# Optimization experiments

Measured on AMD Instinct MI355X. Metric: run time of the kernel, lower is better.

Reference implementation:

```python
import jax, jax.numpy as jnp
import numpy as np

B, P, K = 32, 2048, 20   # events, points per event, kNN neighbors
EPS = 1e-5               # BatchNorm eps (eval mode, running stats)


def setup_inputs() -> dict:
    key = jax.random.key(0)
    ks = iter(jax.random.split(key, 64))
    inp = {}
    inp["x"] = jax.random.normal(next(ks), (B * P, 7), jnp.float32)
    inp["batch"] = jnp.repeat(jnp.arange(B, dtype=jnp.int32), P)

    def add_layer(tag, cin, cout):
        inp["w" + tag] = jax.random.normal(next(ks), (cin, cout), jnp.float32) / np.sqrt(cin)
        inp["b" + tag] = jax.random.normal(next(ks), (cout,), jnp.float32) * 0.01
        inp["g" + tag] = jax.random.uniform(next(ks), (cout,), jnp.float32, 0.5, 1.5)
        inp["e" + tag] = jax.random.normal(next(ks), (cout,), jnp.float32) * 0.1
        inp["m" + tag] = jax.random.normal(next(ks), (cout,), jnp.float32) * 0.1
        inp["v" + tag] = jax.random.uniform(next(ks), (cout,), jnp.float32, 0.5, 1.5)

    # conv1 MLP: [14, 64, 64, 64]
    add_layer("10", 14, 64)
    add_layer("11", 64, 64)
    add_layer("12", 64, 64)
    # conv2 MLP: [128, 128]
    add_layer("20", 128, 128)
    return inp


def _lin_relu_bn(h, W, b, g, be, rm, rv):
    # Linear -> ReLU -> BatchNorm1d (eval mode: running stats)
    h = jax.nn.relu(h @ W + b)
    return (h - rm) * (g / jnp.sqrt(rv + EPS)) + be


def _knn_idx(x):
    # x: [B, P, C] -> indices of K nearest neighbors (incl. self), [B, P, K]
    sq = jnp.sum(x * x, axis=-1)                                   # [B, P]
    d = sq[:, :, None] + sq[:, None, :] - 2.0 * jnp.einsum("bpc,bqc->bpq", x, x)
    _, idx = jax.lax.top_k(-d, K)
    return idx


def _edge_conv(x, mlp):
    # DynamicEdgeConv: kNN graph on current features, edge MLP([x_i, x_j - x_i]), max-aggr
    idx = _knn_idx(x)                                              # [B, P, K]
    xj = jax.vmap(lambda xb, ib: xb[ib])(x, idx)                   # [B, P, K, C]
    xi = jnp.broadcast_to(x[:, :, None, :], xj.shape)
    e = jnp.concatenate([xi, xj - xi], axis=-1)                    # [B, P, K, 2C]
    return jnp.max(mlp(e), axis=2)                                 # [B, P, Cout]


def reference(x, batch,
              w10, b10, g10, e10, m10, v10,
              w11, b11, g11, e11, m11, v11,
              w12, b12, g12, e12, m12, v12,
              w20, b20, g20, e20, m20, v20):
    xb = x.reshape(B, P, -1)                                       # fixed-size events

    def mlp1(e):
        h = _lin_relu_bn(e, w10, b10, g10, e10, m10, v10)
        h = _lin_relu_bn(h, w11, b11, g11, e11, m11, v11)
        return _lin_relu_bn(h, w12, b12, g12, e12, m12, v12)

    def mlp2(e):
        return _lin_relu_bn(e, w20, b20, g20, e20, m20, v20)

    x1 = _edge_conv(xb, mlp1)                                      # [B, P, 64]
    x2 = _edge_conv(x1, mlp2)                                      # [B, P, 128]
    out = jnp.concatenate([x1, x2], axis=-1).reshape(B * P, 192)
    return out, batch
```

## Files before the change

kernel.cpp:

```cpp
#include <hip/hip_runtime.h>

#define B_EV 32
#define P_PT 2048
#define K_NN 20
#define NPTS (B_EV*P_PT)
#define EPS_BN 1e-5f
#define RINF 3.0e38f

typedef _Float16 half8 __attribute__((ext_vector_type(8)));
typedef float f32x4 __attribute__((ext_vector_type(4)));

static constexpr int oWA10=0, oWB10=448, oB10=896, oT10=960,
  oT11=5184,
  oT12=9408,
  oWA20=9472, oWB20=17664, oB20=25856, oT20=25984,
  oB11p=26048, oB12p=26112,
  oW11hi=26176, oW11lo=28224,
  oW12hi=30272, oW12lo=32320;
static constexpr size_t oIDX = 36864;
static constexpr size_t oA1  = 1347584;
static constexpr size_t oB1  = oA1 + (size_t)NPTS*64;
static constexpr size_t oV2  = oB1 + (size_t)NPTS*64;
static constexpr size_t oX1  = oV2 + (size_t)NPTS*128;
static constexpr size_t oSQ  = oX1 + (size_t)NPTS*64;
static constexpr size_t oD   = oSQ + (size_t)NPTS;
static constexpr size_t oU2  = oA1;

__global__ __launch_bounds__(128) void k_prep(
  const float* w10,const float* b10,const float* g10,const float* e10,const float* m10,const float* v10,
  const float* w11,const float* b11,const float* g11,const float* e11,const float* m11,const float* v11,
  const float* w12,const float* b12,const float* g12,const float* e12,const float* m12,const float* v12,
  const float* w20,const float* b20,const float* g20,const float* e20,const float* m20,const float* v20,
  float* ws)
{
  __shared__ float t10s[64], t11s[64];
  int c = threadIdx.x;
  if (c < 64) {
    float s0 = g10[c]*rsqrtf(v10[c]+EPS_BN);
    ws[oB10+c]=b10[c]*s0;
    float t10 = e10[c]-m10[c]*s0; ws[oT10+c]=t10; t10s[c]=t10;
    for (int i=0;i<7;i++){
      ws[oWA10+i*64+c]=(w10[i*64+c]-w10[(7+i)*64+c])*s0;
      ws[oWB10+i*64+c]=w10[(7+i)*64+c]*s0;
    }
    float s1 = g11[c]*rsqrtf(v11[c]+EPS_BN);
    float t11 = e11[c]-m11[c]*s1; ws[oT11+c]=t11; t11s[c]=t11;
    float s2 = g12[c]*rsqrtf(v12[c]+EPS_BN);
    ws[oT12+c]=e12[c]-m12[c]*s2;
  }
  __syncthreads();
  if (c < 64) {
    float s1 = g11[c]*rsqrtf(v11[c]+EPS_BN);
    _Float16* W1hi = (_Float16*)(ws + oW11hi);
    _Float16* W1lo = (_Float16*)(ws + oW11lo);
    float acc = b11[c]*s1;
    for (int i=0;i<64;i++){
      float wv = w11[i*64+c]*s1;
      _Float16 h = (_Float16)wv;
      W1hi[c*64+i] = h;
      W1lo[c*64+i] = (_Float16)(wv - (float)h);
      acc = fmaf(t10s[i], wv, acc);
    }
    ws[oB11p+c]=acc;
    float s2 = g12[c]*rsqrtf(v12[c]+EPS_BN);
    _Float16* W2hi = (_Float16*)(ws + oW12hi);
    _Float16* W2lo = (_Float16*)(ws + oW12lo);
    float acc2 = b12[c]*s2;
    for (int i=0;i<64;i++){
      float wv = w12[i*64+c]*s2;
      _Float16 h = (_Float16)wv;
      W2hi[c*64+i] = h;
      W2lo[c*64+i] = (_Float16)(wv - (float)h);
      acc2 = fmaf(t11s[i], wv, acc2);
    }
    ws[oB12p+c]=acc2;
  }
  {
    float s = g20[c]*rsqrtf(v20[c]+EPS_BN);
    ws[oB20+c]=b20[c]*s; ws[oT20+c]=e20[c]-m20[c]*s;
    for (int i=0;i<64;i++){
      ws[oWA20+i*128+c]=(w20[i*128+c]-w20[(64+i)*128+c])*s;
      ws[oWB20+i*128+c]=w20[(64+i)*128+c]*s;
    }
  }
}

__device__ __forceinline__ void select20(float (&d)[32], int lane, int base, int g,
                                         int* __restrict__ idxout)
{
  float g4[4];
  #pragma unroll
  for (int k=0;k<4;k++){
    float m = d[8*k];
    #pragma unroll
    for (int j=1;j<8;j++) m = fminf(m, d[8*k+j]);
    g4[k]=m;
  }
  float T = 0.f;
  #pragma unroll 1
  for (int pass=0; pass<20; ++pass){
    float m = fminf(fminf(g4[0],g4[1]), fminf(g4[2],g4[3]));
    #pragma unroll
    for (int off=32; off>0; off>>=1) m = fminf(m, __shfl_xor(m, off, 64));
    if (pass==19){ T=m; break; }
    #pragma unroll
    for (int k=0;k<4;k++){
      if (g4[k]==m){
        #pragma unroll
        for (int j=0;j<8;j++) d[8*k+j] = (d[8*k+j]==m) ? RINF : d[8*k+j];
        float mm = d[8*k];
        #pragma unroll
        for (int j=1;j<8;j++) mm = fminf(mm, d[8*k+j]);
        g4[k]=mm;
      }
    }
  }
  int cnt=0;
  #pragma unroll
  for (int j=0;j<32;j++){
    bool take = (d[j]>=RINF) || (d[j]==T);
    unsigned long long mb = __ballot(take);
    if (take){
      int pos = cnt + (int)__popcll(mb & ((1ull<<lane)-1ull));
      if (pos < K_NN) idxout[(size_t)g*K_NN + pos] = base + j*64 + lane;
    }
    cnt += (int)__popcll(mb);
  }
  if (lane==0){
    for (int r=cnt; r<K_NN; ++r) idxout[(size_t)g*K_NN + r] = g;
  }
}

__global__ __launch_bounds__(512) void k_knn1(const float* __restrict__ x, int* __restrict__ idxout)
{
  __shared__ float xs[P_PT*7];
  int t = threadIdx.x;
  int b = blockIdx.x;
  int xcd = b & 7, kk = b >> 3;
  int e = xcd + ((kk >> 8) << 3);
  int blk = kk & 255;
  const float4* src = (const float4*)(x + (size_t)e*P_PT*7);
  #pragma unroll
  for (int u=0;u<7;u++) ((float4*)xs)[u*512+t] = src[u*512+t];
  __syncthreads();
  int lane = t & 63;
  int g = e*P_PT + blk*8 + (t>>6);
  int pin = g & (P_PT-1);
  float xp[7];
  #pragma unroll
  for (int i=0;i<7;i++) xp[i]=xs[pin*7+i];
  float d[32];
  #pragma unroll
  for (int j=0;j<32;j++){
    const float* xq = xs + (j*64+lane)*7;
    float s=0.f;
    #pragma unroll
    for (int i=0;i<7;i++){ float df=xp[i]-xq[i]; s=fmaf(df,df,s); }
    d[j]=s;
  }
  select20(d, lane, e*P_PT, g, idxout);
}

__global__ __launch_bounds__(256) void k_ab1(const float* __restrict__ x, const float* __restrict__ W,
                                             float* __restrict__ A1, float* __restrict__ B1)
{
  int g = blockIdx.x*256+threadIdx.x;
  float xi[7];
  #pragma unroll
  for (int i=0;i<7;i++) xi[i]=x[(size_t)g*7+i];
  float a[64], b[64];
  #pragma unroll
  for (int c=0;c<64;c++){ a[c]=W[oB10+c]; b[c]=0.f; }
  #pragma unroll
  for (int i=0;i<7;i++){
    #pragma unroll
    for (int c=0;c<64;c++) a[c]=fmaf(xi[i], W[oWA10+i*64+c], a[c]);
    #pragma unroll
    for (int c=0;c<64;c++) b[c]=fmaf(xi[i], W[oWB10+i*64+c], b[c]);
  }
  #pragma unroll
  for (int c=0;c<64;c+=4){
    float4 oa; oa.x=a[c]; oa.y=a[c+1]; oa.z=a[c+2]; oa.w=a[c+3];
    *(float4*)(A1+(size_t)g*64+c)=oa;
    float4 ob; ob.x=b[c]; ob.y=b[c+1]; ob.z=b[c+2]; ob.w=b[c+3];
    *(float4*)(B1+(size_t)g*64+c)=ob;
  }
}

__global__ __launch_bounds__(256, 2) void k_ec1m(const int* __restrict__ idx, const float* __restrict__ ws,
    const float* __restrict__ A1, const float* __restrict__ B1,
    float* __restrict__ x1, float* __restrict__ sqv, float* __restrict__ out)
{
  __shared__ _Float16 h2hi[4][32*64];
  __shared__ _Float16 h2lo[4][32*64];
  int t = threadIdx.x, w = t>>6, lane = t&63;
  int b = blockIdx.x;
  int xcd = b & 7, kk = b >> 3;
  int ev = xcd + ((kk >> 9) << 3);
  int i = ev*P_PT + (kk & 511)*4 + w;
  int lg = lane>>4, lr = lane&15;

  int j0 = idx[(size_t)i*K_NN + lr];
  int j1 = (lr < 4) ? idx[(size_t)i*K_NN + 16 + lr] : i;

  const float* Ap  = A1 + (size_t)i*64;
  const float* Bp0 = B1 + (size_t)j0*64;
  const float* Bp1 = B1 + (size_t)j1*64;
  float4 av[2][2], bv[2][2][2];
  #pragma unroll
  for (int ks=0;ks<2;ks++){
    int c0 = ks*32 + lg*8;
    av[ks][0]    = *(const float4*)(Ap +c0);
    av[ks][1]    = *(const float4*)(Ap +c0+4);
    bv[0][ks][0] = *(const float4*)(Bp0+c0);
    bv[0][ks][1] = *(const float4*)(Bp0+c0+4);
    bv[1][ks][0] = *(const float4*)(Bp1+c0);
    bv[1][ks][1] = *(const float4*)(Bp1+c0+4);
  }

  half8 AH[2][2], AL[2][2];
  #pragma unroll
  for (int m=0;m<2;m++){
    #pragma unroll
    for (int ks=0;ks<2;ks++){
      float hv[8];
      hv[0]=fmaxf(av[ks][0].x+bv[m][ks][0].x,0.f);
      hv[1]=fmaxf(av[ks][0].y+bv[m][ks][0].y,0.f);
      hv[2]=fmaxf(av[ks][0].z+bv[m][ks][0].z,0.f);
      hv[3]=fmaxf(av[ks][0].w+bv[m][ks][0].w,0.f);
      hv[4]=fmaxf(av[ks][1].x+bv[m][ks][1].x,0.f);
      hv[5]=fmaxf(av[ks][1].y+bv[m][ks][1].y,0.f);
      hv[6]=fmaxf(av[ks][1].z+bv[m][ks][1].z,0.f);
      hv[7]=fmaxf(av[ks][1].w+bv[m][ks][1].w,0.f);
      half8 ah, al;
      #pragma unroll
      for (int q=0;q<8;q++){
        _Float16 h = (_Float16)hv[q];
        ah[q]=h; al[q]=(_Float16)(hv[q]-(float)h);
      }
      AH[m][ks]=ah; AL[m][ks]=al;
    }
  }

  f32x4 acc[2][4];
  #pragma unroll
  for (int nt=0;nt<4;nt++){
    float bb = ws[oB11p + nt*16 + lr];
    f32x4 v = {bb,bb,bb,bb};
    acc[0][nt]=v; acc[1][nt]=v;
  }
  {
    const _Float16* W1hi = (const _Float16*)(ws + oW11hi);
    const _Float16* W1lo = (const _Float16*)(ws + oW11lo);
    #pragma unroll
    for (int nt=0;nt<4;nt++){
      const _Float16* whp = W1hi + (nt*16+lr)*64 + lg*8;
      const _Float16* wlp = W1lo + (nt*16+lr)*64 + lg*8;
      half8 wh0 = *(const half8*)(whp);
      half8 wh1 = *(const half8*)(whp+32);
      half8 wl0 = *(const half8*)(wlp);
      half8 wl1 = *(const half8*)(wlp+32);
      #pragma unroll
      for (int m=0;m<2;m++){
        acc[m][nt] = __builtin_amdgcn_mfma_f32_16x16x32_f16(AH[m][0], wh0, acc[m][nt], 0,0,0);
        acc[m][nt] = __builtin_amdgcn_mfma_f32_16x16x32_f16(AL[m][0], wh0, acc[m][nt], 0,0,0);
        acc[m][nt] = __builtin_amdgcn_mfma_f32_16x16x32_f16(AH[m][0], wl0, acc[m][nt], 0,0,0);
        acc[m][nt] = __builtin_amdgcn_mfma_f32_16x16x32_f16(AH[m][1], wh1, acc[m][nt], 0,0,0);
        acc[m][nt] = __builtin_amdgcn_mfma_f32_16x16x32_f16(AL[m][1], wh1, acc[m][nt], 0,0,0);
        acc[m][nt] = __builtin_amdgcn_mfma_f32_16x16x32_f16(AH[m][1], wl1, acc[m][nt], 0,0,0);
      }
    }
  }

  _Float16* hbh = h2hi[w];
  _Float16* hbl = h2lo[w];
  #pragma unroll
  for (int m=0;m<2;m++){
    #pragma unroll
    for (int nt=0;nt<4;nt++){
      #pragma unroll
      for (int r=0;r<4;r++){
        int row = m*16 + lg*4 + r;
        int col = nt*16 + lr;
        int baddr = (row*128 + col*2) ^ ((row&7)<<4);
        float v = fmaxf(acc[m][nt][r], 0.f);
        _Float16 vh = (_Float16)v;
        *(_Float16*)((char*)hbh + baddr) = vh;
        *(_Float16*)((char*)hbl + baddr) = (_Float16)(v-(float)vh);
      }
    }
  }

  half8 AH2[2][2], AL2[2][2];
  #pragma unroll
  for (int m=0;m<2;m++){
    #pragma unroll
    for (int ks=0;ks<2;ks++){
      int row = m*16 + lr;
      int baddr = (row*128 + (ks*32 + lg*8)*2) ^ ((row&7)<<4);
      AH2[m][ks] = *(const half8*)((char*)hbh + baddr);
      AL2[m][ks] = *(const half8*)((char*)hbl + baddr);
    }
  }

  f32x4 acc2[2][4];
  #pragma unroll
  for (int nt=0;nt<4;nt++){
    float bb = ws[oB12p + nt*16 + lr];
    f32x4 v = {bb,bb,bb,bb};
    acc2[0][nt]=v; acc2[1][nt]=v;
  }
  {
    const _Float16* W2hi = (const _Float16*)(ws + oW12hi);
    const _Float16* W2lo = (const _Float16*)(ws + oW12lo);
    #pragma unroll
    for (int nt=0;nt<4;nt++){
      const _Float16* whp = W2hi + (nt*16+lr)*64 + lg*8;
      const _Float16* wlp = W2lo + (nt*16+lr)*64 + lg*8;
      half8 wh0 = *(const half8*)(whp);
      half8 wh1 = *(const half8*)(whp+32);
      half8 wl0 = *(const half8*)(wlp);
      half8 wl1 = *(const half8*)(wlp+32);
      #pragma unroll
      for (int m=0;m<2;m++){
        acc2[m][nt] = __builtin_amdgcn_mfma_f32_16x16x32_f16(AH2[m][0], wh0, acc2[m][nt], 0,0,0);
        acc2[m][nt] = __builtin_amdgcn_mfma_f32_16x16x32_f16(AL2[m][0], wh0, acc2[m][nt], 0,0,0);
        acc2[m][nt] = __builtin_amdgcn_mfma_f32_16x16x32_f16(AH2[m][0], wl0, acc2[m][nt], 0,0,0);
        acc2[m][nt] = __builtin_amdgcn_mfma_f32_16x16x32_f16(AH2[m][1], wh1, acc2[m][nt], 0,0,0);
        acc2[m][nt] = __builtin_amdgcn_mfma_f32_16x16x32_f16(AL2[m][1], wh1, acc2[m][nt], 0,0,0);
        acc2[m][nt] = __builtin_amdgcn_mfma_f32_16x16x32_f16(AH2[m][1], wl1, acc2[m][nt], 0,0,0);
      }
    }
  }

  float fin[4]; float sq = 0.f;
  #pragma unroll
  for (int nt=0;nt<4;nt++){
    float cv = -RINF;
    #pragma unroll
    for (int r=0;r<4;r++) cv = fmaxf(cv, acc2[0][nt][r]);
    if (lg==0){
      #pragma unroll
      for (int r=0;r<4;r++) cv = fmaxf(cv, acc2[1][nt][r]);
    }
    cv = fmaxf(cv, __shfl_xor(cv,16,64));
    cv = fmaxf(cv, __shfl_xor(cv,32,64));
    fin[nt] = fmaxf(cv, 0.f) + ws[oT12 + nt*16 + lr];
    sq = fmaf(fin[nt], fin[nt], sq);
  }
  if (lane < 16){
    #pragma unroll
    for (int nt=0;nt<4;nt++){
      x1[(size_t)i*64 + nt*16 + lane] = fin[nt];
      out[(size_t)i*192 + nt*16 + lane] = fin[nt];
    }
  }
  #pragma unroll
  for (int off=1; off<16; off<<=1) sq += __shfl_xor(sq, off, 64);
  if (lane == 0) sqv[i] = sq;
}

__global__ __launch_bounds__(256) void k_dist2(const float* __restrict__ x1, const float* __restrict__ sqv,
                                               float* __restrict__ D, int e0, int ce)
{
  __shared__ float As[64][68], Bs[64][68];
  int b = blockIdx.x;
  int z, inner;
  if (ce == 8){ z = b & 7; inner = b >> 3; }
  else        { z = b / 1024; inner = b % 1024; }
  int by = inner >> 5, bx = inner & 31;
  int e = e0 + z;
  const float* Xe = x1 + (size_t)e*P_PT*64;
  int rb = by*64, cb = bx*64;
  int t = threadIdx.x;
  int tr = t>>4, tk=(t&15)*4;
  #pragma unroll
  for (int rr=0;rr<4;rr++){
    int r = tr + 16*rr;
    float4 va = *(const float4*)(Xe + (size_t)(rb+r)*64 + tk);
    As[tk][r]=va.x; As[tk+1][r]=va.y; As[tk+2][r]=va.z; As[tk+3][r]=va.w;
    float4 vb = *(const float4*)(Xe + (size_t)(cb+r)*64 + tk);
    Bs[tk][r]=vb.x; Bs[tk+1][r]=vb.y; Bs[tk+2][r]=vb.z; Bs[tk+3][r]=vb.w;
  }
  __syncthreads();
  int tx=t&15, ty=t>>4;
  float acc[4][4];
  #pragma unroll
  for (int i=0;i<4;i++){
    #pragma unroll
    for (int j=0;j<4;j++) acc[i][j]=0.f;
  }
  #pragma unroll 4
  for (int k=0;k<64;k++){
    float4 a4 = *(const float4*)(&As[k][ty*4]);
    float4 b4 = *(const float4*)(&Bs[k][tx*4]);
    float a0=a4.x, a1=a4.y, a2=a4.z, a3=a4.w;
    float b0=b4.x, b1=b4.y, b2=b4.z, b3=b4.w;
    acc[0][0]=fmaf(a0,b0,acc[0][0]); acc[0][1]=fmaf(a0,b1,acc[0][1]);
    acc[0][2]=fmaf(a0,b2,acc[0][2]); acc[0][3]=fmaf(a0,b3,acc[0][3]);
    acc[1][0]=fmaf(a1,b0,acc[1][0]); acc[1][1]=fmaf(a1,b1,acc[1][1]);
    acc[1][2]=fmaf(a1,b2,acc[1][2]); acc[1][3]=fmaf(a1,b3,acc[1][3]);
    acc[2][0]=fmaf(a2,b0,acc[2][0]); acc[2][1]=fmaf(a2,b1,acc[2][1]);
    acc[2][2]=fmaf(a2,b2,acc[2][2]); acc[2][3]=fmaf(a2,b3,acc[2][3]);
    acc[3][0]=fmaf(a3,b0,acc[3][0]); acc[3][1]=fmaf(a3,b1,acc[3][1]);
    acc[3][2]=fmaf(a3,b2,acc[3][2]); acc[3][3]=fmaf(a3,b3,acc[3][3]);
  }
  float sr[4], sc[4];
  #pragma unroll
  for (int i=0;i<4;i++){ sr[i]=sqv[e*P_PT + rb+ty*4+i]; sc[i]=sqv[e*P_PT + cb+tx*4+i]; }
  #pragma unroll
  for (int i=0;i<4;i++){
    float4 o;
    o.x = sr[i]+sc[0]-2.f*acc[i][0];
    o.y = sr[i]+sc[1]-2.f*acc[i][1];
    o.z = sr[i]+sc[2]-2.f*acc[i][2];
    o.w = sr[i]+sc[3]-2.f*acc[i][3];
    *(float4*)(D + (size_t)(z*P_PT + rb+ty*4+i)*P_PT + cb + tx*4) = o;
  }
}

__global__ __launch_bounds__(256) void k_sel2(const float* __restrict__ D, int* __restrict__ idxout, int e0)
{
  int t=threadIdx.x, lane=t&63;
  int pl = blockIdx.x*4 + (t>>6);
  int le = pl>>11, pin = pl&(P_PT-1);
  int e = e0 + le;
  int g = e*P_PT + pin;
  const float* Dr = D + (size_t)pl*P_PT;
  float d[32];
  #pragma unroll
  for (int j=0;j<32;j++) d[j]=Dr[j*64+lane];
  select20(d, lane, e*P_PT, g, idxout);
}

__global__ __launch_bounds__(256) void k_uv2(const float* __restrict__ x1, const float* __restrict__ W,
                                             float* __restrict__ U2, float* __restrict__ V2)
{
  int g = blockIdx.x*256 + threadIdx.x;
  int half = blockIdx.y & 1;
  bool isU = blockIdx.y < 2;
  const float* Wb = W + (isU?oWA20:oWB20) + half*64;
  float acc[64];
  #pragma unroll
  for (int c=0;c<64;c++) acc[c] = isU ? W[oB20+half*64+c] : 0.f;
  const float* xp = x1 + (size_t)g*64;
  #pragma unroll 1
  for (int i=0;i<64;i+=4){
    float4 xv = *(const float4*)(xp+i);
    #pragma unroll
    for (int c=0;c<64;c++) acc[c]=fmaf(xv.x, Wb[(i+0)*128+c], acc[c]);
    #pragma unroll
    for (int c=0;c<64;c++) acc[c]=fmaf(xv.y, Wb[(i+1)*128+c], acc[c]);
    #pragma unroll
    for (int c=0;c<64;c++) acc[c]=fmaf(xv.z, Wb[(i+2)*128+c], acc[c]);
    #pragma unroll
    for (int c=0;c<64;c++) acc[c]=fmaf(xv.w, Wb[(i+3)*128+c], acc[c]);
  }
  float* dst = (isU?U2:V2) + (size_t)g*128 + half*64;
  #pragma unroll
  for (int c=0;c<64;c+=4){
    float4 o; o.x=acc[c]; o.y=acc[c+1]; o.z=acc[c+2]; o.w=acc[c+3];
    *(float4*)(dst+c)=o;
  }
}

__global__ __launch_bounds__(256) void k_gather2(const int* __restrict__ idx, const float* __restrict__ U2,
     const float* __restrict__ V2, const float* __restrict__ W, float* __restrict__ out)
{
  int b = blockIdx.x;
  int xcd = b & 7, kk = b >> 3;
  int ev = xcd + ((kk >> 3) << 3);
  int g = ev*P_PT + (kk & 7)*256 + threadIdx.x;
  int half = blockIdx.y;
  float mx[64];
  #pragma unroll
  for (int c=0;c<64;c++) mx[c]=-RINF;
  for (int k=0;k<K_NN;k++){
    int j = idx[(size_t)g*K_NN+k];
    const float4* vp = (const float4*)(V2 + (size_t)j*128 + half*64);
    #pragma unroll
    for (int c4=0;c4<16;c4++){
      float4 v=vp[c4];
      mx[c4*4+0]=fmaxf(mx[c4*4+0],v.x);
      mx[c4*4+1]=fmaxf(mx[c4*4+1],v.y);
      mx[c4*4+2]=fmaxf(mx[c4*4+2],v.z);
      mx[c4*4+3]=fmaxf(mx[c4*4+3],v.w);
    }
  }
  const float* Up = U2 + (size_t)g*128 + half*64;
  float* op = out + (size_t)g*192 + 64 + half*64;
  #pragma unroll
  for (int c=0;c<64;c+=4){
    float4 o;
    o.x = fmaxf(Up[c+0]+mx[c+0],0.f)+W[oT20+half*64+c+0];
    o.y = fmaxf(Up[c+1]+mx[c+1],0.f)+W[oT20+half*64+c+1];
    o.z = fmaxf(Up[c+2]+mx[c+2],0.f)+W[oT20+half*64+c+2];
    o.w = fmaxf(Up[c+3]+mx[c+3],0.f)+W[oT20+half*64+c+3];
    *(float4*)(op+c)=o;
  }
}

__global__ __launch_bounds__(256) void k_batchf(const int* __restrict__ batch, float* __restrict__ out){
  int i = blockIdx.x*256+threadIdx.x;
  out[(size_t)NPTS*192 + i] = (float)batch[i];
}

extern "C" void kernel_launch(void* const* d_in, const int* in_sizes, int n_in,
                              void* d_out, int out_size, void* d_ws, size_t ws_size,
                              hipStream_t stream)
{
  const float* x     = (const float*)d_in[0];
  const int*   batch = (const int*)d_in[1];
  const float* w10=(const float*)d_in[2],  *b10=(const float*)d_in[3],  *g10=(const float*)d_in[4],
             *e10=(const float*)d_in[5],  *m10=(const float*)d_in[6],  *v10=(const float*)d_in[7];
  const float* w11=(const float*)d_in[8],  *b11=(const float*)d_in[9],  *g11=(const float*)d_in[10],
             *e11=(const float*)d_in[11], *m11=(const float*)d_in[12], *v11=(const float*)d_in[13];
  const float* w12=(const float*)d_in[14], *b12=(const float*)d_in[15], *g12=(const float*)d_in[16],
             *e12=(const float*)d_in[17], *m12=(const float*)d_in[18], *v12=(const float*)d_in[19];
  const float* w20=(const float*)d_in[20], *b20=(const float*)d_in[21], *g20=(const float*)d_in[22],
             *e20=(const float*)d_in[23], *m20=(const float*)d_in[24], *v20=(const float*)d_in[25];

  float* ws  = (float*)d_ws;
  float* out = (float*)d_out;
  int*   idxp = (int*)(ws + oIDX);

  k_prep<<<1,128,0,stream>>>(w10,b10,g10,e10,m10,v10, w11,b11,g11,e11,m11,v11,
                             w12,b12,g12,e12,m12,v12, w20,b20,g20,e20,m20,v20, ws);
  k_knn1<<<NPTS/8, 512, 0, stream>>>(x, idxp);
  k_ab1<<<NPTS/256, 256, 0, stream>>>(x, ws, ws+oA1, ws+oB1);
  k_ec1m<<<NPTS/4, 256, 0, stream>>>(idxp, ws, ws+oA1, ws+oB1, ws+oX1, ws+oSQ, out);

  size_t wsFloats = ws_size/4;
  long avail = (long)wsFloats - (long)oD;
  int CE = (int)(avail / (2048L*2048L));
  if (CE < 1) CE = 1;
  if (CE > 8) CE = 8;
  for (int e0=0; e0<B_EV; e0+=CE){
    int ce = (B_EV - e0 < CE) ? (B_EV - e0) : CE;
    k_dist2<<<ce*1024,256,0,stream>>>(ws+oX1, ws+oSQ, ws+oD, e0, ce);
    k_sel2<<<ce*512,256,0,stream>>>(ws+oD, idxp, e0);
  }

  k_uv2<<<dim3(NPTS/256,4),256,0,stream>>>(ws+oX1, ws, ws+oU2, ws+oV2);
  k_gather2<<<dim3(NPTS/256,2),256,0,stream>>>(idxp, ws+oU2, ws+oV2, ws, out);
  k_batchf<<<NPTS/256,256,0,stream>>>(batch, out);
}
```

Measured before the change: 1.171 ms.

## Pack two points' 40 edges into three MFMA row tiles per wavefront

Each wavefront in the edge-conv-1 MLP kernel now processes two points instead of one. Their 40 neighbor edges are packed into three 16-row MFMA tiles instead of two half-empty tiles per point, which cuts wasted padding rows from 12 of 32 to 8 of 48. The intermediate activations are now staged in LDS as fp32 and split into hi/lo fp16 on readback, rather than stored as two fp16 arrays. The grid is halved. The cost is more registers per thread and a larger shared buffer, which may lower occupancy.

Result: faster. 1.064 ms (-9.2%).

```diff
diff --git a/kernel.cpp b/kernel.cpp
--- a/kernel.cpp
+++ b/kernel.cpp
@@ -191,63 +191,73 @@
     const float* __restrict__ A1, const float* __restrict__ B1,
     float* __restrict__ x1, float* __restrict__ sqv, float* __restrict__ out)
 {
-  __shared__ _Float16 h2hi[4][32*64];
-  __shared__ _Float16 h2lo[4][32*64];
+  __shared__ float h2s[4][48*64];
   int t = threadIdx.x, w = t>>6, lane = t&63;
   int b = blockIdx.x;
   int xcd = b & 7, kk = b >> 3;
-  int ev = xcd + ((kk >> 9) << 3);
-  int i = ev*P_PT + (kk & 511)*4 + w;
+  int ev = xcd + ((kk >> 8) << 3);
+  int iA = ev*P_PT + (kk & 255)*8 + w*2;
+  int iB = iA + 1;
   int lg = lane>>4, lr = lane&15;
 
-  int j0 = idx[(size_t)i*K_NN + lr];
-  int j1 = (lr < 4) ? idx[(size_t)i*K_NN + 16 + lr] : i;
-
-  const float* Ap  = A1 + (size_t)i*64;
-  const float* Bp0 = B1 + (size_t)j0*64;
-  const float* Bp1 = B1 + (size_t)j1*64;
-  float4 av[2][2], bv[2][2][2];
+  int jT0 = idx[(size_t)iA*K_NN + lr];
+  int jT1 = idx[(size_t)iB*K_NN + lr];
+  int a2 = (lr < 4) ? iA*K_NN + 16 + lr : iB*K_NN + 12 + lr;
+  a2 = (lr < 8) ? a2 : 0;
+  int jT2 = (lr < 8) ? idx[a2] : iA;
+
+  const float* ApA = A1 + (size_t)iA*64;
+  const float* ApB = A1 + (size_t)iB*64;
+  float4 avA[2][2], avB[2][2], bv[3][2][2];
+  const float* Bp0 = B1 + (size_t)jT0*64;
+  const float* Bp1 = B1 + (size_t)jT1*64;
+  const float* Bp2 = B1 + (size_t)jT2*64;
   #pragma unroll
   for (int ks=0;ks<2;ks++){
     int c0 = ks*32 + lg*8;
-    av[ks][0]    = *(const float4*)(Ap +c0);
-    av[ks][1]    = *(const float4*)(Ap +c0+4);
-    bv[0][ks][0] = *(const float4*)(Bp0+c0);
-    bv[0][ks][1] = *(const float4*)(Bp0+c0+4);
-    bv[1][ks][0] = *(const float4*)(Bp1+c0);
-    bv[1][ks][1] = *(const float4*)(Bp1+c0+4);
-  }
-
-  half8 AH[2][2], AL[2][2];
-  #pragma unroll
-  for (int m=0;m<2;m++){
+    avA[ks][0] = *(const float4*)(ApA+c0); avA[ks][1] = *(const float4*)(ApA+c0+4);
+    avB[ks][0] = *(const float4*)(ApB+c0); avB[ks][1] = *(const float4*)(ApB+c0+4);
+    bv[0][ks][0] = *(const float4*)(Bp0+c0); bv[0][ks][1] = *(const float4*)(Bp0+c0+4);
+    bv[1][ks][0] = *(const float4*)(Bp1+c0); bv[1][ks][1] = *(const float4*)(Bp1+c0+4);
+    bv[2][ks][0] = *(const float4*)(Bp2+c0); bv[2][ks][1] = *(const float4*)(Bp2+c0+4);
+  }
+
+  bool useB2 = (lr >= 4) && (lr < 8);
+  half8 AH[3][2], AL[3][2];
+  #pragma unroll
+  for (int tile=0;tile<3;tile++){
     #pragma unroll
     for (int ks=0;ks<2;ks++){
+      float4 a0, a1;
+      if (tile==0){ a0 = avA[ks][0]; a1 = avA[ks][1]; }
+      else if (tile==1){ a0 = avB[ks][0]; a1 = avB[ks][1]; }
+      else {
+        a0.x = useB2 ? avB[ks][0].x : avA[ks][0].x;  a0.y = useB2 ? avB[ks][0].y : avA[ks][0].y;
+        a0.z = useB2 ? avB[ks][0].z : avA[ks][0].z;  a0.w = useB2 ? avB[ks][0].w : avA[ks][0].w;
+        a1.x = useB2 ? avB[ks][1].x : avA[ks][1].x;  a1.y = useB2 ? avB[ks][1].y : avA[ks][1].y;
+        a1.z = useB2 ? avB[ks][1].z : avA[ks][1].z;  a1.w = useB2 ? avB[ks][1].w : avA[ks][1].w;
+      }
       float hv[8];
-      hv[0]=fmaxf(av[ks][0].x+bv[m][ks][0].x,0.f);
-      hv[1]=fmaxf(av[ks][0].y+bv[m][ks][0].y,0.f);
-      hv[2]=fmaxf(av[ks][0].z+bv[m][ks][0].z,0.f);
-      hv[3]=fmaxf(av[ks][0].w+bv[m][ks][0].w,0.f);
-      hv[4]=fmaxf(av[ks][1].x+bv[m][ks][1].x,0.f);
-      hv[5]=fmaxf(av[ks][1].y+bv[m][ks][1].y,0.f);
-      hv[6]=fmaxf(av[ks][1].z+bv[m][ks][1].z,0.f);
-      hv[7]=fmaxf(av[ks][1].w+bv[m][ks][1].w,0.f);
+      hv[0]=fmaxf(a0.x+bv[tile][ks][0].x,0.f); hv[1]=fmaxf(a0.y+bv[tile][ks][0].y,0.f);
+      hv[2]=fmaxf(a0.z+bv[tile][ks][0].z,0.f); hv[3]=fmaxf(a0.w+bv[tile][ks][0].w,0.f);
+      hv[4]=fmaxf(a1.x+bv[tile][ks][1].x,0.f); hv[5]=fmaxf(a1.y+bv[tile][ks][1].y,0.f);
+      hv[6]=fmaxf(a1.z+bv[tile][ks][1].z,0.f); hv[7]=fmaxf(a1.w+bv[tile][ks][1].w,0.f);
       half8 ah, al;
       #pragma unroll
       for (int q=0;q<8;q++){
         _Float16 h = (_Float16)hv[q];
         ah[q]=h; al[q]=(_Float16)(hv[q]-(float)h);
       }
-      AH[m][ks]=ah; AL[m][ks]=al;
-    }
-  }
-
-  f32x4 acc[2][4];
+      AH[tile][ks]=ah; AL[tile][ks]=al;
+    }
+  }
+
+  f32x4 acc[3][4];
   #pragma unroll
   for (int nt=0;nt<4;nt++){
     float bb = ws[oB11p + nt*16 + lr];
     f32x4 v = {bb,bb,bb,bb};
-    acc[0][nt]=v; acc[1][nt]=v;
+    acc[0][nt]=v; acc[1][nt]=v; acc[2][nt]=v;
   }
   {
     const _Float16* W1hi = (const _Float16*)(ws + oW11hi);
@@ -261,54 +271,63 @@
       half8 wl0 = *(const half8*)(wlp);
       half8 wl1 = *(const half8*)(wlp+32);
       #pragma unroll
-      for (int m=0;m<2;m++){
-        acc[m][nt] = __builtin_amdgcn_mfma_f32_16x16x32_f16(AH[m][0], wh0, acc[m][nt], 0,0,0);
-        acc[m][nt] = __builtin_amdgcn_mfma_f32_16x16x32_f16(AL[m][0], wh0, acc[m][nt], 0,0,0);
-        acc[m][nt] = __builtin_amdgcn_mfma_f32_16x16x32_f16(AH[m][0], wl0, acc[m][nt], 0,0,0);
-        acc[m][nt] = __builtin_amdgcn_mfma_f32_16x16x32_f16(AH[m][1], wh1, acc[m][nt], 0,0,0);
-        acc[m][nt] = __builtin_amdgcn_mfma_f32_16x16x32_f16(AL[m][1], wh1, acc[m][nt], 0,0,0);
-        acc[m][nt] = __builtin_amdgcn_mfma_f32_16x16x32_f16(AH[m][1], wl1, acc[m][nt], 0,0,0);
-      }
-    }
-  }
-
-  _Float16* hbh = h2hi[w];
-  _Float16* hbl = h2lo[w];
-  #pragma unroll
-  for (int m=0;m<2;m++){
+      for (int tile=0;tile<3;tile++){
+        acc[tile][nt] = __builtin_amdgcn_mfma_f32_16x16x32_f16(AH[tile][0], wh0, acc[tile][nt], 0,0,0);
+        acc[tile][nt] = __builtin_amdgcn_mfma_f32_16x16x32_f16(AL[tile][0], wh0, acc[tile][nt], 0,0,0);
+        acc[tile][nt] = __builtin_amdgcn_mfma_f32_16x16x32_f16(AH[tile][0], wl0, acc[tile][nt], 0,0,0);
+        acc[tile][nt] = __builtin_amdgcn_mfma_f32_16x16x32_f16(AH[tile][1], wh1, acc[tile][nt], 0,0,0);
+        acc[tile][nt] = __builtin_amdgcn_mfma_f32_16x16x32_f16(AL[tile][1], wh1, acc[tile][nt], 0,0,0);
+        acc[tile][nt] = __builtin_amdgcn_mfma_f32_16x16x32_f16(AH[tile][1], wl1, acc[tile][nt], 0,0,0);
+      }
+    }
+  }
+
+  float* hb = h2s[w];
+  #pragma unroll
+  for (int tile=0;tile<3;tile++){
     #pragma unroll
     for (int nt=0;nt<4;nt++){
       #pragma unroll
       for (int r=0;r<4;r++){
-        int row = m*16 + lg*4 + r;
+        int row = tile*16 + lg*4 + r;
         int col = nt*16 + lr;
-        int baddr = (row*128 + col*2) ^ ((row&7)<<4);
-        float v = fmaxf(acc[m][nt][r], 0.f);
-        _Float16 vh = (_Float16)v;
-        *(_Float16*)((char*)hbh + baddr) = vh;
-        *(_Float16*)((char*)hbl + baddr) = (_Float16)(v-(float)vh);
-      }
-    }
-  }
-
-  half8 AH2[2][2], AL2[2][2];
-  #pragma unroll
-  for (int m=0;m<2;m++){
+        int baddr = (row*256 + col*4) ^ ((row&7)<<4);
+        *(float*)((char*)hb + baddr) = fmaxf(acc[tile][nt][r], 0.f);
+      }
+    }
+  }
+
+  half8 AH2[3][2], AL2[3][2];
+  #pragma unroll
+  for (int tile=0;tile<3;tile++){
     #pragma unroll
     for (int ks=0;ks<2;ks++){
-      int row = m*16 + lr;
-      int baddr = (row*128 + (ks*32 + lg*8)*2) ^ ((row&7)<<4);
-      AH2[m][ks] = *(const half8*)((char*)hbh + baddr);
-      AL2[m][ks] = *(const half8*)((char*)hbl + baddr);
-    }
-  }
-
-  f32x4 acc2[2][4];
+      int row = tile*16 + lr;
+      int byte0 = (row*256 + (ks*32 + lg*8)*4);
+      int s = (row&7)<<4;
+      f32x4 v0 = *(const f32x4*)((char*)hb + ((byte0)^s));
+      f32x4 v1 = *(const f32x4*)((char*)hb + ((byte0+16)^s));
+      half8 ah, al;
+      #pragma unroll
+      for (int q=0;q<4;q++){
+        _Float16 h = (_Float16)v0[q];
+        ah[q]=h; al[q]=(_Float16)(v0[q]-(float)h);
+      }
+      #pragma unroll
+      for (int q=0;q<4;q++){
+        _Float16 h = (_Float16)v1[q];
+        ah[4+q]=h; al[4+q]=(_Float16)(v1[q]-(float)h);
+      }
+      AH2[tile][ks]=ah; AL2[tile][ks]=al;
+    }
+  }
+
+  f32x4 acc2[3][4];
   #pragma unroll
   for (int nt=0;nt<4;nt++){
     float bb = ws[oB12p + nt*16 + lr];
     f32x4 v = {bb,bb,bb,bb};
-    acc2[0][nt]=v; acc2[1][nt]=v;
+    acc2[0][nt]=v; acc2[1][nt]=v; acc2[2][nt]=v;
   }
   {
     const _Float16* W2hi = (const _Float16*)(ws + oW12hi);
@@ -322,42 +341,60 @@
       half8 wl0 = *(const half8*)(wlp);
       half8 wl1 = *(const half8*)(wlp+32);
       #pragma unroll
-      for (int m=0;m<2;m++){
-        acc2[m][nt] = __builtin_amdgcn_mfma_f32_16x16x32_f16(AH2[m][0], wh0, acc2[m][nt], 0,0,0);
-        acc2[m][nt] = __builtin_amdgcn_mfma_f32_16x16x32_f16(AL2[m][0], wh0, acc2[m][nt], 0,0,0);
-        acc2[m][nt] = __builtin_amdgcn_mfma_f32_16x16x32_f16(AH2[m][0], wl0, acc2[m][nt], 0,0,0);
-        acc2[m][nt] = __builtin_amdgcn_mfma_f32_16x16x32_f16(AH2[m][1], wh1, acc2[m][nt], 0,0,0);
-        acc2[m][nt] = __builtin_amdgcn_mfma_f32_16x16x32_f16(AL2[m][1], wh1, acc2[m][nt], 0,0,0);
-        acc2[m][nt] = __builtin_amdgcn_mfma_f32_16x16x32_f16(AH2[m][1], wl1, acc2[m][nt], 0,0,0);
-      }
-    }
-  }
-
-  float fin[4]; float sq = 0.f;
+      for (int tile=0;tile<3;tile++){
+        acc2[tile][nt] = __builtin_amdgcn_mfma_f32_16x16x32_f16(AH2[tile][0], wh0, acc2[tile][nt], 0,0,0);
+        acc2[tile][nt] = __builtin_amdgcn_mfma_f32_16x16x32_f16(AL2[tile][0], wh0, acc2[tile][nt], 0,0,0);
+        acc2[tile][nt] = __builtin_amdgcn_mfma_f32_16x16x32_f16(AH2[tile][0], wl0, acc2[tile][nt], 0,0,0);
+        acc2[tile][nt] = __builtin_amdgcn_mfma_f32_16x16x32_f16(AH2[tile][1], wh1, acc2[tile][nt], 0,0,0);
+        acc2[tile][nt] = __builtin_amdgcn_mfma_f32_16x16x32_f16(AL2[tile][1], wh1, acc2[tile][nt], 0,0,0);
+        acc2[tile][nt] = __builtin_amdgcn_mfma_f32_16x16x32_f16(AH2[tile][1], wl1, acc2[tile][nt], 0,0,0);
+      }
+    }
+  }
+
+  float finA[4], finB[4];
+  float sqA = 0.f, sqB = 0.f;
   #pragma unroll
   for (int nt=0;nt<4;nt++){
-    float cv = -RINF;
-    #pragma unroll
-    for (int r=0;r<4;r++) cv = fmaxf(cv, acc2[0][nt][r]);
+    float cvA = -RINF;
+    #pragma unroll
+    for (int r=0;r<4;r++) cvA = fmaxf(cvA, acc2[0][nt][r]);
     if (lg==0){
       #pragma unroll
-      for (int r=0;r<4;r++) cv = fmaxf(cv, acc2[1][nt][r]);
-    }
-    cv = fmaxf(cv, __shfl_xor(cv,16,64));
-    cv = fmaxf(cv, __shfl_xor(cv,32,64));
-    fin[nt] = fmaxf(cv, 0.f) + ws[oT12 + nt*16 + lr];
-    sq = fmaf(fin[nt], fin[nt], sq);
+      for (int r=0;r<4;r++) cvA = fmaxf(cvA, acc2[2][nt][r]);
+    }
+    cvA = fmaxf(cvA, __shfl_xor(cvA,16,64));
+    cvA = fmaxf(cvA, __shfl_xor(cvA,32,64));
+    finA[nt] = fmaxf(cvA, 0.f) + ws[oT12 + nt*16 + lr];
+    sqA = fmaf(finA[nt], finA[nt], sqA);
+
+    float cvB = -RINF;
+    #pragma unroll
+    for (int r=0;r<4;r++) cvB = fmaxf(cvB, acc2[1][nt][r]);
+    if (lg==1){
+      #pragma unroll
+      for (int r=0;r<4;r++) cvB = fmaxf(cvB, acc2[2][nt][r]);
+    }
+    cvB = fmaxf(cvB, __shfl_xor(cvB,16,64));
+    cvB = fmaxf(cvB, __shfl_xor(cvB,32,64));
+    finB[nt] = fmaxf(cvB, 0.f) + ws[oT12 + nt*16 + lr];
+    sqB = fmaf(finB[nt], finB[nt], sqB);
   }
   if (lane < 16){
     #pragma unroll
     for (int nt=0;nt<4;nt++){
-      x1[(size_t)i*64 + nt*16 + lane] = fin[nt];
-      out[(size_t)i*192 + nt*16 + lane] = fin[nt];
-    }
-  }
-  #pragma unroll
-  for (int off=1; off<16; off<<=1) sq += __shfl_xor(sq, off, 64);
-  if (lane == 0) sqv[i] = sq;
+      x1[(size_t)iA*64 + nt*16 + lane] = finA[nt];
+      out[(size_t)iA*192 + nt*16 + lane] = finA[nt];
+      x1[(size_t)iB*64 + nt*16 + lane] = finB[nt];
+      out[(size_t)iB*192 + nt*16 + lane] = finB[nt];
+    }
+  }
+  #pragma unroll
+  for (int off=1; off<16; off<<=1){
+    sqA += __shfl_xor(sqA, off, 64);
+    sqB += __shfl_xor(sqB, off, 64);
+  }
+  if (lane == 0){ sqv[iA] = sqA; sqv[iB] = sqB; }
 }
 
 __global__ __launch_bounds__(256) void k_dist2(const float* __restrict__ x1, const float* __restrict__ sqv,
@@ -528,7 +565,7 @@
                              w12,b12,g12,e12,m12,v12, w20,b20,g20,e20,m20,v20, ws);
   k_knn1<<<NPTS/8, 512, 0, stream>>>(x, idxp);
   k_ab1<<<NPTS/256, 256, 0, stream>>>(x, ws, ws+oA1, ws+oB1);
-  k_ec1m<<<NPTS/4, 256, 0, stream>>>(idxp, ws, ws+oA1, ws+oB1, ws+oX1, ws+oSQ, out);
+  k_ec1m<<<NPTS/8, 256, 0, stream>>>(idxp, ws, ws+oA1, ws+oB1, ws+oX1, ws+oSQ, out);
 
   size_t wsFloats = ws_size/4;
   long avail = (long)wsFloats - (long)oD;
```
